# Optimization experiments

Measured on AMD Instinct MI355X. Metric: run time of the kernel, lower is better.

Reference implementation:

```python
import jax, jax.numpy as jnp
import numpy as np

FACTOR = 5


def setup_inputs() -> dict:
    key = jax.random.key(0)
    k1, k2, k3, k4 = jax.random.split(key, 4)
    B, L, H, D = 4, 2048, 8, 64
    sample_k = min(FACTOR * int(np.ceil(np.log(L))), L)  # 40
    return {
        "query": jax.random.normal(k1, (B, L, H, D), dtype=jnp.float32),
        "key": jax.random.normal(k2, (B, L, H, D), dtype=jnp.float32),
        "value": jax.random.normal(k3, (B, L, H, D), dtype=jnp.float32),
        "index_sample": jax.random.randint(k4, (L, sample_k), 0, L, dtype=jnp.int32),
    }


def reference(query, key, value, index_sample):
    # query/key/value: (B, L, H, D); mask_flag=True, output_attention=False
    B, L_Q, H, D = query.shape
    L_K = key.shape[1]
    q = jnp.swapaxes(query, 1, 2)  # (B,H,L_Q,D)
    k = jnp.swapaxes(key, 1, 2)    # (B,H,L_K,D)
    v = jnp.swapaxes(value, 1, 2)  # (B,H,L_K,D)

    U_part = min(FACTOR * int(np.ceil(np.log(L_K))), L_K)  # sample_k
    u = min(FACTOR * int(np.ceil(np.log(L_Q))), L_Q)       # n_top

    # --- _prob_QK: sampled QK scores, sparsity measure M, top-u queries ---
    # K_sample: gather sample_k keys per query position -> (B,H,L_Q,sample_k,D)
    K_sample = k[:, :, index_sample, :]
    Q_K_sample = jnp.einsum("bhid,bhisd->bhis", q, K_sample)  # (B,H,L_Q,sample_k)
    M = Q_K_sample.max(axis=-1) - Q_K_sample.sum(axis=-1) / L_K  # (B,H,L_Q)
    _, M_top = jax.lax.top_k(M, u)  # (B,H,u) indices of selected queries

    Q_reduce = jnp.take_along_axis(q, M_top[..., None], axis=2)  # (B,H,u,D)
    scores = jnp.einsum("bhud,bhkd->bhuk", Q_reduce, k)          # (B,H,u,L_K)

    scale = 1.0 / jnp.sqrt(jnp.float32(D))
    scores = scores * scale

    # --- initial context: causal cumsum of V (mask_flag=True) ---
    context = jnp.cumsum(v, axis=2)  # (B,H,L_Q,D)

    # --- update context: causal ProbMask on selected rows, softmax, scatter ---
    # mask[b,h,t,kk] = kk > M_top[b,h,t]
    mask = jnp.arange(L_K)[None, None, None, :] > M_top[..., None]
    scores = jnp.where(mask, -jnp.inf, scores)
    attn = jax.nn.softmax(scores, axis=-1)
    ctx_upd = jnp.einsum("bhuk,bhkd->bhud", attn, v)  # (B,H,u,D)

    b_idx = jnp.arange(context.shape[0])[:, None, None]
    h_idx = jnp.arange(context.shape[1])[None, :, None]
    context = context.at[b_idx, h_idx, M_top].set(ctx_upd)

    return jnp.swapaxes(context, 1, 2)  # (B, L_Q, H, D)
```

## Files before the change

### kernel.cpp

```cpp
#include <hip/hip_runtime.h>
#include <hip/hip_bf16.h>
#include <math.h>

constexpr int B = 4;
constexpr int L = 2048;
constexpr int H = 8;
constexpr int D = 64;
constexpr int S = 40;
constexpr int U = 40;
constexpr int C = 32;
constexpr int CHUNK = L / C;
constexpr int NSEG = 16;
constexpr int SEG  = L / NSEG;

__global__ void fused_Mpart(const float* __restrict__ q,
                            const float* __restrict__ k,
                            const float* __restrict__ v,
                            const int*   __restrict__ samp,
                            float* __restrict__ M,
                            float* __restrict__ part) {
    __shared__ float pa[H * 680];
    int tid = threadIdx.x;

    if (blockIdx.x < 256) {
        int idx = blockIdx.x * 256 + tid;
        int b   = idx >> 14;
        int rem = idx & 16383;
        int c   = rem >> 9;
        int hd  = rem & 511;
        const float* base = v + ((size_t)(b * L + c * CHUNK) * H * D) + hd;
        float s = 0.f;
        for (int i = 0; i < CHUNK; i++) s += base[(size_t)i * (H * D)];
        int h = hd >> 6, d = hd & 63;
        part[((size_t)(b * H + h) * C + c) * D + d] = s;
        return;
    }

    int blk = blockIdx.x - 256;
    int xcd = blk & 7;
    int b   = xcd >> 1;
    int l   = ((blk >> 3) << 1) | (xcd & 1);
    int h      = tid >> 5;
    int lane32 = tid & 31;
    int g  = lane32 >> 4;
    int d4 = lane32 & 15;

    const float4 qv = *(const float4*)(q + ((size_t)(b * L + l) * H + h) * D + d4 * 4);
    const int* srow = samp + l * S;
    float* pah = pa + h * 680;

#pragma unroll 4
    for (int sb = 0; sb < S; sb += 2) {
        int i0 = srow[sb];
        int i1 = srow[sb + 1];
        int idx = g ? i1 : i0;
        int s = sb + g;
        float4 kv = *(const float4*)(k + ((size_t)(b * L + idx) * H + h) * D + d4 * 4);
        pah[s * 17 + d4] = qv.x * kv.x + qv.y * kv.y + qv.z * kv.z + qv.w * kv.w;
    }
    __syncthreads();

    int s1 = lane32;
    float t0 = 0.f, t1 = 0.f, t2 = 0.f, t3 = 0.f;
#pragma unroll
    for (int i = 0; i < 16; i += 4) {
        t0 += pah[s1 * 17 + i];
        t1 += pah[s1 * 17 + i + 1];
        t2 += pah[s1 * 17 + i + 2];
        t3 += pah[s1 * 17 + i + 3];
    }
    float dot1 = (t0 + t1) + (t2 + t3);
    float mv = dot1, sv = dot1;
    if (lane32 < S - 32) {
        int s2 = 32 + lane32;
        float u0 = 0.f, u1 = 0.f, u2 = 0.f, u3 = 0.f;
#pragma unroll
        for (int i = 0; i < 16; i += 4) {
            u0 += pah[s2 * 17 + i];
            u1 += pah[s2 * 17 + i + 1];
            u2 += pah[s2 * 17 + i + 2];
            u3 += pah[s2 * 17 + i + 3];
        }
        float dot2 = (u0 + u1) + (u2 + u3);
        mv = fmaxf(mv, dot2);
        sv += dot2;
    }
#pragma unroll
    for (int off = 1; off <= 16; off <<= 1) {
        mv = fmaxf(mv, __shfl_xor(mv, off));
        sv += __shfl_xor(sv, off);
    }
    if (lane32 == 0) M[(size_t)(b * H + h) * L + l] = mv - sv * (1.0f / (float)L);
}

__global__ void fused_topk_cumsum(const float* __restrict__ M,
                                  const float* __restrict__ v,
                                  const float* __restrict__ part,
                                  int* __restrict__ Mtop,
                                  float* __restrict__ out) {
    int tid = threadIdx.x;

    if (blockIdx.x >= 32) {
        int idx = (blockIdx.x - 32) * 256 + tid;
        int b   = idx >> 14;
        int rem = idx & 16383;
        int c   = rem >> 9;
        int hd  = rem & 511;
        int h = hd >> 6, d = hd & 63;

        float run = 0.f;
        for (int cc = 0; cc < c; cc++)
            run += part[((size_t)(b * H + h) * C + cc) * D + d];

        const float* base  = v   + ((size_t)(b * L + c * CHUNK) * H * D) + hd;
        float*       obase = out + ((size_t)(b * L + c * CHUNK) * H * D) + hd;
        for (int i = 0; i < CHUNK; i++) {
            run += base[(size_t)i * (H * D)];
            obase[(size_t)i * (H * D)] = run;
        }
        return;
    }

    int bh = blockIdx.x;
    const float4* row4 = (const float4*)(M + (size_t)bh * L);
    float4 v0 = row4[tid * 2];
    float4 v1 = row4[tid * 2 + 1];
    float vals[8] = {v0.x, v0.y, v0.z, v0.w, v1.x, v1.y, v1.z, v1.w};
    int base = tid * 8;

    __shared__ float wv[4];
    __shared__ int   wi[4];
    __shared__ int   bidx;

    float lbv = vals[0];
    int   lbi = base;
#pragma unroll
    for (int r = 1; r < 8; r++)
        if (vals[r] > lbv) { lbv = vals[r]; lbi = base + r; }

    for (int it = 0; it < U; it++) {
        float bv = lbv;
        int   bi = lbi;
#pragma unroll
        for (int off = 1; off <= 32; off <<= 1) {
            float ov = __shfl_xor(bv, off);
            int   oi = __shfl_xor(bi, off);
            if (ov > bv || (ov == bv && oi < bi)) { bv = ov; bi = oi; }
        }
        int w = tid >> 6;
        if ((tid & 63) == 0) { wv[w] = bv; wi[w] = bi; }
        __syncthreads();
        if (tid == 0) {
            float Bv = wv[0]; int Bi = wi[0];
#pragma unroll
            for (int ww = 1; ww < 4; ww++)
                if (wv[ww] > Bv || (wv[ww] == Bv && wi[ww] < Bi)) { Bv = wv[ww]; Bi = wi[ww]; }
            Mtop[bh * U + it] = Bi;
            bidx = Bi;
        }
        __syncthreads();
        int kb = bidx;
        if (kb >= base && kb < base + 8) {
#pragma unroll
            for (int r = 0; r < 8; r++)
                if (base + r == kb) vals[r] = -INFINITY;
            lbv = vals[0]; lbi = base;
#pragma unroll
            for (int r = 1; r < 8; r++)
                if (vals[r] > lbv) { lbv = vals[r]; lbi = base + r; }
        }
    }
}

__global__ __launch_bounds__(256, 2)
void attn_batched(const float* __restrict__ q,
                  const float* __restrict__ k,
                  const float* __restrict__ v,
                  const int*   __restrict__ Mtop,
                  float* __restrict__ ml,
                  float* __restrict__ pacc) {
    int blk = blockIdx.x;
    int xcd = blk & 7;
    int b   = xcd >> 1;
    int r   = ((blk >> 3) << 1) | (xcd & 1);
    int h   = r >> 4;
    int seg = r & 15;
    int bh  = b * H + h;
    int j0  = seg * SEG;
    int tid = threadIdx.x;

    __shared__ float Qs[U * D];
    __shared__ float KV[SEG * D];
    __shared__ float Sc[U * SEG];
    __shared__ float red[U * 4];
    __shared__ float mrow[U];
    __shared__ int   qis[U];

    if (tid < U) qis[tid] = Mtop[bh * U + tid];
    __syncthreads();

    for (int i = tid; i < U * 16; i += 256) {
        int u = i >> 4, d4 = i & 15;
        *(float4*)&Qs[u * D + d4 * 4] =
            *(const float4*)(q + ((size_t)(b * L + qis[u]) * H + h) * D + d4 * 4);
    }
    for (int i = tid; i < SEG * 16; i += 256) {
        int rr = i >> 4, d4 = i & 15;
        float4 kv = *(const float4*)(k + ((size_t)(b * L + j0 + rr) * H + h) * D + d4 * 4);
        *(float4*)&KV[rr * D + (d4 ^ (rr & 15)) * 4] = kv;
    }
    __syncthreads();

    int ug = tid >> 5;
    int jg = tid & 31;
    int jlow = jg & 15;
    float acc[5][4];
#pragma unroll
    for (int uu = 0; uu < 5; uu++)
#pragma unroll
        for (int jj = 0; jj < 4; jj++) acc[uu][jj] = 0.f;

#pragma unroll
    for (int kk4 = 0; kk4 < 16; kk4++) {
        float4 kf[4];
        int slot = kk4 ^ jlow;
#pragma unroll
        for (int jj = 0; jj < 4; jj++)
            kf[jj] = *(const float4*)&KV[(jg + 32 * jj) * D + slot * 4];
#pragma unroll
        for (int uu = 0; uu < 5; uu++) {
            float4 qf = *(const float4*)&Qs[(ug * 5 + uu) * D + kk4 * 4];
#pragma unroll
            for (int jj = 0; jj < 4; jj++) {
                acc[uu][jj] += qf.x * kf[jj].x + qf.y * kf[jj].y
                             + qf.z * kf[jj].z + qf.w * kf[jj].w;
            }
        }
    }
#pragma unroll
    for (int uu = 0; uu < 5; uu++) {
        int u = ug * 5 + uu;
        int um = u & 15;
#pragma unroll
        for (int jj = 0; jj < 4; jj++) {
            int j = jg + 32 * jj;
            Sc[u * SEG + 4 * ((j >> 2) ^ um) + (j & 3)] = acc[uu][jj] * 0.125f;
        }
    }
    __syncthreads();

    for (int i = tid; i < SEG * 16; i += 256) {
        int rr = i >> 4, d4 = i & 15;
        float4 vv = *(const float4*)(v + ((size_t)(b * L + j0 + rr) * H + h) * D + d4 * 4);
        *(float4*)&KV[rr * D + (d4 ^ (rr & 15)) * 4] = vv;
    }

    int su = tid >> 2, sq = tid & 3;
    int nkc = 0;
    if (tid < U * 4) {
        int nk = qis[su] + 1 - j0;
        nkc = nk < 0 ? 0 : (nk > SEG ? SEG : nk);
        int um = su & 15;
        float mvx = -INFINITY;
        for (int t = 0; t < 32; t++) {
            int i = sq + 4 * t;
            if (i < nkc) mvx = fmaxf(mvx, Sc[su * SEG + 4 * ((i >> 2) ^ um) + (i & 3)]);
        }
        red[su * 4 + sq] = mvx;
    }
    __syncthreads();
    if (tid < U) {
        float m = fmaxf(fmaxf(red[tid * 4], red[tid * 4 + 1]),
                        fmaxf(red[tid * 4 + 2], red[tid * 4 + 3]));
        mrow[tid] = m;
    }
    __syncthreads();
    if (tid < U * 4) {
        float m = mrow[su];
        int um = su & 15;
        float ls = 0.f;
        for (int t = 0; t < 32; t++) {
            int i = sq + 4 * t;
            int addr = su * SEG + 4 * ((i >> 2) ^ um) + (i & 3);
            float e = 0.f;
            if (i < nkc) e = __expf(Sc[addr] - m);
            Sc[addr] = e;
            ls += e;
        }
        red[su * 4 + sq] = ls;
    }
    __syncthreads();
    if (tid < U) {
        float ls = (red[tid * 4] + red[tid * 4 + 1]) + (red[tid * 4 + 2] + red[tid * 4 + 3]);
        size_t mli = 2 * ((size_t)(bh * U + tid) * NSEG + seg);
        ml[mli]     = mrow[tid];
        ml[mli + 1] = ls;
    }

    int vg = jg;
    float a2[5][2];
#pragma unroll
    for (int uu = 0; uu < 5; uu++) { a2[uu][0] = 0.f; a2[uu][1] = 0.f; }

    for (int j4 = 0; j4 < 32; j4++) {
        float4 pf[5];
#pragma unroll
        for (int uu = 0; uu < 5; uu++) {
            int u = ug * 5 + uu;
            pf[uu] = *(const float4*)&Sc[u * SEG + 4 * (j4 ^ (u & 15))];
        }
#pragma unroll
        for (int jj = 0; jj < 4; jj++) {
            int j = j4 * 4 + jj;
            int fo = 4 * ((vg >> 1) ^ (j & 15)) + ((2 * vg) & 3);
            float2 vv = *(const float2*)&KV[j * D + fo];
#pragma unroll
            for (int uu = 0; uu < 5; uu++) {
                float p = ((const float*)&pf[uu])[jj];
                a2[uu][0] += p * vv.x;
                a2[uu][1] += p * vv.y;
            }
        }
    }
#pragma unroll
    for (int uu = 0; uu < 5; uu++) {
        int u = ug * 5 + uu;
        float2 w2 = make_float2(a2[uu][0], a2[uu][1]);
        *(float2*)&pacc[((size_t)(bh * U + u) * NSEG + seg) * D + 2 * vg] = w2;
    }
}

__global__ void attn_combine(const int* __restrict__ Mtop,
                             const float* __restrict__ ml,
                             const float* __restrict__ pacc,
                             float* __restrict__ out) {
    int blk = blockIdx.x;
    int u  = blk % U;
    int bh = blk / U;
    int h  = bh % H;
    int b  = bh / H;
    int d  = threadIdx.x;
    int qi = Mtop[bh * U + u];

    size_t r0 = (size_t)blk * NSEG;
    float m = -INFINITY;
#pragma unroll
    for (int s = 0; s < NSEG; s++) m = fmaxf(m, ml[2 * (r0 + s)]);

    float lt = 0.f, acc = 0.f;
#pragma unroll
    for (int s = 0; s < NSEG; s++) {
        float ms = ml[2 * (r0 + s)];
        float w  = __expf(ms - m);
        lt  += ml[2 * (r0 + s) + 1] * w;
        acc += pacc[(r0 + s) * D + d] * w;
    }
    out[((size_t)(b * L + qi) * H + h) * D + d] = acc / lt;
}

extern "C" void kernel_launch(void* const* d_in, const int* in_sizes, int n_in,
                              void* d_out, int out_size, void* d_ws, size_t ws_size,
                              hipStream_t stream) {
    const float* q    = (const float*)d_in[0];
    const float* k    = (const float*)d_in[1];
    const float* v    = (const float*)d_in[2];
    const int*   samp = (const int*)d_in[3];
    float* out = (float*)d_out;

    float* M    = (float*)d_ws;
    int*   Mtop = (int*)(M + (size_t)B * H * L);
    float* part = (float*)(Mtop + (size_t)B * H * U);
    float* ml   = part + (size_t)B * H * C * D;
    float* pacc = ml + (size_t)B * H * U * NSEG * 2;

    fused_Mpart<<<256 + B * L, 256, 0, stream>>>(q, k, v, samp, M, part);
    fused_topk_cumsum<<<32 + 256, 256, 0, stream>>>(M, v, part, Mtop, out);
    attn_batched<<<B * H * NSEG, 256, 0, stream>>>(q, k, v, Mtop, ml, pacc);
    attn_combine<<<B * H * U, 64, 0, stream>>>(Mtop, ml, pacc, out);
}
```

Baseline: 187.0 us.

## Rewrite top-k as single-wavefront packed-key selection extracting two maxima per round

The top-k selection now runs in one 64-thread wavefront per (b,h) row. Each lane owns 32 values, encoded as order-preserving unsigned keys packed with an inverted index. The lanes track a top-2 pair and merge it with 64-bit shuffles, so two winners come out per round with no shared memory or __syncthreads, removing the block-level barriers and halving the number of reduction rounds. The cumsum half is relaunched with 64-thread blocks to fit the new block size. The shared-memory stride and the sample-loop unroll factor also change, adding register pressure from the 32-value arrays and the 64-bit shuffles.

```diff
diff --git a/kernel.cpp b/kernel.cpp
--- a/kernel.cpp
+++ b/kernel.cpp
@@ -12,6 +12,7 @@
 constexpr int CHUNK = L / C;
 constexpr int NSEG = 16;
 constexpr int SEG  = L / NSEG;
+constexpr int PAH  = 688;
 
 __global__ void fused_Mpart(const float* __restrict__ q,
                             const float* __restrict__ k,
@@ -19,7 +20,7 @@
                             const int*   __restrict__ samp,
                             float* __restrict__ M,
                             float* __restrict__ part) {
-    __shared__ float pa[H * 680];
+    __shared__ float pa[H * PAH];
     int tid = threadIdx.x;
 
     if (blockIdx.x < 256) {
@@ -47,9 +48,9 @@
 
     const float4 qv = *(const float4*)(q + ((size_t)(b * L + l) * H + h) * D + d4 * 4);
     const int* srow = samp + l * S;
-    float* pah = pa + h * 680;
-
-#pragma unroll 4
+    float* pah = pa + h * PAH;
+
+#pragma unroll 10
     for (int sb = 0; sb < S; sb += 2) {
         int i0 = srow[sb];
         int i1 = srow[sb + 1];
@@ -101,7 +102,7 @@
     int tid = threadIdx.x;
 
     if (blockIdx.x >= 32) {
-        int idx = (blockIdx.x - 32) * 256 + tid;
+        int idx = (blockIdx.x - 32) * 64 + tid;
         int b   = idx >> 14;
         int rem = idx & 16383;
         int c   = rem >> 9;
@@ -121,53 +122,65 @@
         return;
     }
 
-    int bh = blockIdx.x;
-    const float4* row4 = (const float4*)(M + (size_t)bh * L);
-    float4 v0 = row4[tid * 2];
-    float4 v1 = row4[tid * 2 + 1];
-    float vals[8] = {v0.x, v0.y, v0.z, v0.w, v1.x, v1.y, v1.z, v1.w};
-    int base = tid * 8;
-
-    __shared__ float wv[4];
-    __shared__ int   wi[4];
-    __shared__ int   bidx;
-
-    float lbv = vals[0];
-    int   lbi = base;
-#pragma unroll
-    for (int r = 1; r < 8; r++)
-        if (vals[r] > lbv) { lbv = vals[r]; lbi = base + r; }
-
-    for (int it = 0; it < U; it++) {
-        float bv = lbv;
-        int   bi = lbi;
-#pragma unroll
-        for (int off = 1; off <= 32; off <<= 1) {
-            float ov = __shfl_xor(bv, off);
-            int   oi = __shfl_xor(bi, off);
-            if (ov > bv || (ov == bv && oi < bi)) { bv = ov; bi = oi; }
-        }
-        int w = tid >> 6;
-        if ((tid & 63) == 0) { wv[w] = bv; wi[w] = bi; }
-        __syncthreads();
+    int bh   = blockIdx.x;
+    int base = tid * 32;
+    const float* row = M + (size_t)bh * L;
+
+    unsigned int vals[32];
+#pragma unroll
+    for (int r4 = 0; r4 < 8; r4++) {
+        float4 f = *(const float4*)(row + base + r4 * 4);
+        const float ff[4] = {f.x, f.y, f.z, f.w};
+#pragma unroll
+        for (int j = 0; j < 4; j++) {
+            unsigned int i = __float_as_uint(ff[j]);
+            vals[r4 * 4 + j] = (i & 0x80000000u) ? ~i : (i | 0x80000000u);
+        }
+    }
+
+    unsigned long long k1 = 0ull, k2 = 0ull;
+#pragma unroll
+    for (int r = 0; r < 32; r++) {
+        unsigned long long kk =
+            ((unsigned long long)vals[r] << 32) | (unsigned int)~(base + r);
+        if (kk > k1) { k2 = k1; k1 = kk; }
+        else if (kk > k2) { k2 = kk; }
+    }
+
+    for (int it = 0; it < U; it += 2) {
+        unsigned long long a1 = k1, a2 = k2;
+#pragma unroll
+        for (int off = 1; off < 64; off <<= 1) {
+            unsigned long long o1 = __shfl_xor(a1, off);
+            unsigned long long o2 = __shfl_xor(a2, off);
+            unsigned long long hi = a1 > o1 ? a1 : o1;
+            unsigned long long lo = a1 > o1 ? o1 : a1;
+            unsigned long long ss = a2 > o2 ? a2 : o2;
+            a1 = hi;
+            a2 = lo > ss ? lo : ss;
+        }
+        int i1 = (int)~(unsigned int)a1;
+        int i2 = (int)~(unsigned int)a2;
         if (tid == 0) {
-            float Bv = wv[0]; int Bi = wi[0];
-#pragma unroll
-            for (int ww = 1; ww < 4; ww++)
-                if (wv[ww] > Bv || (wv[ww] == Bv && wi[ww] < Bi)) { Bv = wv[ww]; Bi = wi[ww]; }
-            Mtop[bh * U + it] = Bi;
-            bidx = Bi;
-        }
-        __syncthreads();
-        int kb = bidx;
-        if (kb >= base && kb < base + 8) {
-#pragma unroll
-            for (int r = 0; r < 8; r++)
-                if (base + r == kb) vals[r] = -INFINITY;
-            lbv = vals[0]; lbi = base;
-#pragma unroll
-            for (int r = 1; r < 8; r++)
-                if (vals[r] > lbv) { lbv = vals[r]; lbi = base + r; }
+            Mtop[bh * U + it]     = i1;
+            Mtop[bh * U + it + 1] = i2;
+        }
+        bool own1 = (i1 >> 5) == tid;
+        bool own2 = (i2 >> 5) == tid;
+        if (own1 | own2) {
+            int r1 = own1 ? (i1 & 31) : 32;
+            int r2 = own2 ? (i2 & 31) : 32;
+#pragma unroll
+            for (int r = 0; r < 32; r++)
+                if (r == r1 || r == r2) vals[r] = 0u;
+            k1 = 0ull; k2 = 0ull;
+#pragma unroll
+            for (int r = 0; r < 32; r++) {
+                unsigned long long kk =
+                    ((unsigned long long)vals[r] << 32) | (unsigned int)~(base + r);
+                if (kk > k1) { k2 = k1; k1 = kk; }
+                else if (kk > k2) { k2 = kk; }
+            }
         }
     }
 }
@@ -374,7 +387,7 @@
     float* pacc = ml + (size_t)B * H * U * NSEG * 2;
 
     fused_Mpart<<<256 + B * L, 256, 0, stream>>>(q, k, v, samp, M, part);
-    fused_topk_cumsum<<<32 + 256, 256, 0, stream>>>(M, v, part, Mtop, out);
+    fused_topk_cumsum<<<32 + 1024, 64, 0, stream>>>(M, v, part, Mtop, out);
     attn_batched<<<B * H * NSEG, 256, 0, stream>>>(q, k, v, Mtop, ml, pacc);
     attn_combine<<<B * H * U, 64, 0, stream>>>(Mtop, ml, pacc, out);
 }
```

Result: no change. 184.2 us (-1.5%).
